# Performance work log

Hardware: AMD Instinct MI355X
Metric: run time of the kernel (lower is better)

## Reference

```python
import jax, jax.numpy as jnp
import numpy as np

# ---- config (YOLOv4-style, TRAIN_SIZE=608, P2..P5) ----
STRIDES = (4.0, 8.0, 16.0, 32.0)
ANCHORS = np.array([
    [[12, 16], [19, 36], [40, 28], [36, 75]],
    [[36, 75], [76, 55], [72, 146], [142, 110]],
    [[72, 146], [142, 110], [192, 243], [459, 401]],
    [[142, 110], [192, 243], [300, 300], [459, 401]],
], dtype=np.float32)  # [LEVELS, NUM_ANCHORS, 2]
MAX_PROP = 100
SCORE_THRESH = 0.25
IOU_THRESH = 0.5


def decode_prediction(p, anchors, stride):
    # p: [b, A, h, w, 6] -> [b, A*h*w, 5] with xyxy + score
    b, A, h, w, _ = p.shape
    txy, twh, conf, cls = p[..., :2], p[..., 2:4], p[..., 4:5], p[..., 5:6]
    gx, gy = jnp.meshgrid(jnp.arange(w, dtype=p.dtype), jnp.arange(h, dtype=p.dtype))
    grid = jnp.stack([gx, gy], axis=-1)[None, None]  # [1,1,h,w,2]
    xy = (jax.nn.sigmoid(txy) + grid) * stride
    wh = jnp.exp(twh) * anchors[None, :, None, None, :]
    score = jax.nn.sigmoid(conf) * jax.nn.sigmoid(cls)
    x1y1 = xy - 0.5 * wh
    x2y2 = xy + 0.5 * wh
    out = jnp.concatenate([x1y1, x2y2, score], axis=-1)  # [b,A,h,w,5]
    return out.reshape(b, A * h * w, 5)


def _iou_one_vs_all(box, boxes):
    # box: [4], boxes: [N,4] (xyxy)
    lt = jnp.maximum(box[:2], boxes[:, :2])
    rb = jnp.minimum(box[2:], boxes[:, 2:])
    wh = jnp.maximum(rb - lt, 0.0)
    inter = wh[:, 0] * wh[:, 1]
    a1 = jnp.maximum(box[2] - box[0], 0.0) * jnp.maximum(box[3] - box[1], 0.0)
    a2 = jnp.maximum(boxes[:, 2] - boxes[:, 0], 0.0) * jnp.maximum(boxes[:, 3] - boxes[:, 1], 0.0)
    return inter / (a1 + a2 - inter + 1e-9)


def _nms_single(boxes, scores):
    # greedy NMS, padded to MAX_PROP with zero rows
    s0 = jnp.where(scores >= SCORE_THRESH, scores, 0.0)

    def step(s, _):
        i = jnp.argmax(s)
        sc = s[i]
        box = boxes[i]
        keep = sc > 0.0
        row = jnp.where(keep, jnp.concatenate([box, sc[None]]), jnp.zeros(5, boxes.dtype))
        iou = _iou_one_vs_all(box, boxes)
        s = jnp.where((iou > IOU_THRESH) & keep, 0.0, s)
        s = s.at[i].set(0.0)
        return s, row

    _, props = jax.lax.scan(step, s0, None, length=MAX_PROP)
    return props  # [MAX_PROP, 5]


def entry_stop_gradients(t, mask):
    # gradient flows only through entries where mask==1
    return jax.lax.stop_gradient(t) * (1.0 - mask) + t * mask


def _forward(p2, p3, p4, p5):
    anchors = jnp.asarray(ANCHORS)
    d2 = decode_prediction(p2, anchors[0], STRIDES[0])
    d3 = decode_prediction(p3, anchors[1], STRIDES[1])
    d4 = decode_prediction(p4, anchors[2], STRIDES[2])
    d5 = decode_prediction(p5, anchors[3], STRIDES[3])
    proposals = jnp.concatenate([d2, d3, d4, d5], axis=1)  # [b, N, 5]
    proposals = jax.vmap(lambda pr: _nms_single(pr[:, :4], pr[:, 4]))(proposals)  # [b, MAX_PROP, 5]
    mask = (jnp.sum(proposals[..., :4], axis=-1) != 0.0).astype(proposals.dtype)[..., None]
    return entry_stop_gradients(proposals, mask)


def setup_inputs() -> dict:
    key = jax.random.key(0)
    k2, k3, k4, k5 = jax.random.split(key, 4)
    b, A, ch = 32, 4, 6
    return {
        "p2": jax.random.normal(k2, (b, A, 152, 152, ch), dtype=jnp.float32),
        "p3": jax.random.normal(k3, (b, A, 76, 76, ch), dtype=jnp.float32),
        "p4": jax.random.normal(k4, (b, A, 38, 38, ch), dtype=jnp.float32),
        "p5": jax.random.normal(k5, (b, A, 19, 19, ch), dtype=jnp.float32),
    }


def reference(p2, p3, p4, p5):
    return _forward(p2, p3, p4, p5)
```

## Files before the change

kernel.cpp:

```cpp
#include <hip/hip_runtime.h>
#include <cstdint>
#include <cstddef>

typedef unsigned int u32;
typedef unsigned long long u64;

#define NTOT 122740
#define NPAIR 61370
#define KTOP 1024
#define WIN  256
#define NBIN 4096
#define SCORE_T 0.25f
#define TBITS 0x3E800000u

#define RT0 0x3F5DF000u
#define RT1 0x3F3FF000u
#define RT2 0x3F1FF000u
#define RT3 0x3EFFF000u

#define CSTRIDE 128
#define CAP0 4096
#define CAP1 8192
#define CAP2 12288
#define CAP3 16384
#define CAP4 16384
#define OFF0 0
#define OFF1 4096
#define OFF2 12288
#define OFF3 24576
#define OFF4 40960
#define BATCH_ENT 57344

#define F4TOT 184110
#define F4B3 138624
#define F4B4 173280
#define F4B5 181944

#define F4_PER_BLK 3072

#define WS_CAND 16384

__device__ __forceinline__ float sigm(float x) { return 1.0f / (1.0f + expf(-x)); }

__device__ __forceinline__ int score_bin(u32 bits) {
  return min(4095, 1 + (int)((bits - TBITS) >> 12));
}

__device__ __forceinline__ u64 shfl_u64(u64 x, int src) {
  int lo = __shfl((int)(u32)x, src, 64);
  int hi = __shfl((int)(u32)(x >> 32), src, 64);
  return ((u64)(u32)hi << 32) | (u32)lo;
}

__device__ __forceinline__ void score_pair(int P, int b,
    const float* __restrict__ p2, const float* __restrict__ p3,
    const float* __restrict__ p4, const float* __restrict__ p5,
    u32& b0, u32& b1, u32& gi0, u32& gi1)
{
  int t0 = 2 * P;
  const float* p; int l0, LN;
  if (t0 < 92416)       { p = p2; l0 = t0;          LN = 92416; }
  else if (t0 < 115520) { p = p3; l0 = t0 - 92416;  LN = 23104; }
  else if (t0 < 121296) { p = p4; l0 = t0 - 115520; LN = 5776;  }
  else                  { p = p5; l0 = t0 - 121296; LN = 1444;  }
  const float* q = p + ((size_t)b * LN + (size_t)l0) * 6;
  float4 v1 = *(const float4*)(q + 4);
  float4 v2 = *(const float4*)(q + 8);
  float s0 = sigm(v1.x) * sigm(v1.y);
  float s1 = sigm(v2.z) * sigm(v2.w);
  b0 = (s0 >= SCORE_T) ? __float_as_uint(s0) : 0u;
  b1 = (s1 >= SCORE_T) ? __float_as_uint(s1) : 0u;
  gi0 = (u32)t0; gi1 = (u32)(t0 + 1);
}

__device__ float4 decode_box_from_gidx(u32 gidx, int b,
    const float* __restrict__ p2, const float* __restrict__ p3,
    const float* __restrict__ p4, const float* __restrict__ p5)
{
  const float* p; int t, H, W; float stride;
  float aw0, ah0, aw1, ah1, aw2, ah2, aw3, ah3;
  if (gidx < 92416u) {
    p = p2 + (size_t)b * 92416 * 6; t = (int)gidx; H = 152; W = 152; stride = 4.0f;
    aw0=12.f; ah0=16.f; aw1=19.f; ah1=36.f; aw2=40.f; ah2=28.f; aw3=36.f; ah3=75.f;
  } else if (gidx < 115520u) {
    p = p3 + (size_t)b * 23104 * 6; t = (int)(gidx - 92416u); H = 76; W = 76; stride = 8.0f;
    aw0=36.f; ah0=75.f; aw1=76.f; ah1=55.f; aw2=72.f; ah2=146.f; aw3=142.f; ah3=110.f;
  } else if (gidx < 121296u) {
    p = p4 + (size_t)b * 5776 * 6; t = (int)(gidx - 115520u); H = 38; W = 38; stride = 16.0f;
    aw0=72.f; ah0=146.f; aw1=142.f; ah1=110.f; aw2=192.f; ah2=243.f; aw3=459.f; ah3=401.f;
  } else {
    p = p5 + (size_t)b * 1444 * 6; t = (int)(gidx - 121296u); H = 19; W = 19; stride = 32.0f;
    aw0=142.f; ah0=110.f; aw1=192.f; ah1=243.f; aw2=300.f; ah2=300.f; aw3=459.f; ah3=401.f;
  }
  int HW = H * W;
  int a = t / HW;
  int r = t - a * HW;
  int y = r / W;
  int x = r - y * W;
  const float* q = p + (size_t)t * 6;
  float2 t01 = *(const float2*)(q + 0);
  float2 t23 = *(const float2*)(q + 2);
  float cx = (sigm(t01.x) + (float)x) * stride;
  float cy = (sigm(t01.y) + (float)y) * stride;
  float aw = (a == 0) ? aw0 : (a == 1) ? aw1 : (a == 2) ? aw2 : aw3;
  float ah = (a == 0) ? ah0 : (a == 1) ? ah1 : (a == 2) ? ah2 : ah3;
  float bw = expf(t23.x) * aw;
  float bh = expf(t23.y) * ah;
  return make_float4(cx - 0.5f * bw, cy - 0.5f * bh, cx + 0.5f * bw, cy + 0.5f * bh);
}

__device__ __forceinline__ bool iou_gt(float4 A, float4 B) {
  float ltx = fmaxf(A.x, B.x), lty = fmaxf(A.y, B.y);
  float rbx = fminf(A.z, B.z), rby = fminf(A.w, B.w);
  float w = fmaxf(rbx - ltx, 0.0f), h = fmaxf(rby - lty, 0.0f);
  float inter = w * h;
  float a1 = fmaxf(A.z - A.x, 0.0f) * fmaxf(A.w - A.y, 0.0f);
  float a2 = fmaxf(B.z - B.x, 0.0f) * fmaxf(B.w - B.y, 0.0f);
  float iou = inter / (a1 + a2 - inter + 1e-9f);
  return iou > 0.5f;
}

__global__ __launch_bounds__(512)
void decode_kernel(const float* __restrict__ p2, const float* __restrict__ p3,
                   const float* __restrict__ p4, const float* __restrict__ p5,
                   u32* __restrict__ counters, uint2* __restrict__ cand)
{
  __shared__ uint2 stg[2048];
  __shared__ u32 lcnt[8], lseg[8], lrank[8], gbase[8];
  const int tid = threadIdx.x;
  const int b = blockIdx.y;
  if (tid < 8) { lcnt[tid] = 0u; lrank[tid] = 0u; gbase[tid] = 0u; }
  __syncthreads();

  const float4* q2 = (const float4*)p2;
  const float4* q3 = (const float4*)p3;
  const float4* q4 = (const float4*)p4;
  const float4* q5 = (const float4*)p5;
  const int FS = blockIdx.x * F4_PER_BLK;

  u32 kb[6]; u32 kg6[6]; int kr6[6];
  #pragma unroll
  for (int k = 0; k < 6; ++k) {
    kb[k] = 0u; kr6[k] = -1; kg6[k] = 0u;
    int i4 = FS + k * 512 + tid;
    if (i4 < F4TOT) {
      const float4* src;
      if (i4 < F4B3)      src = q2 + (size_t)b * 138624 + i4;
      else if (i4 < F4B4) src = q3 + (size_t)b * 34656  + (i4 - F4B3);
      else if (i4 < F4B5) src = q4 + (size_t)b * 8664   + (i4 - F4B4);
      else                src = q5 + (size_t)b * 2166   + (i4 - F4B5);
      float4 v = *src;
      int k3 = i4 / 3;
      int trib = i4 - 3 * k3;
      if (trib) {
        float cf = (trib == 1) ? v.x : v.z;
        float cl = (trib == 1) ? v.y : v.w;
        float s = sigm(cf) * sigm(cl);
        if (s >= SCORE_T) {
          u32 bb = __float_as_uint(s);
          int r;
          if      (bb >= RT0) r = 0;
          else if (bb >= RT1) r = 1;
          else if (bb >= RT2) r = 2;
          else if (bb >= RT3) r = 3;
          else                r = 4;
          kb[k] = bb; kr6[k] = r;
          kg6[k] = (u32)(2 * k3 + (trib - 1));
          atomicAdd(&lcnt[r], 1u);
        }
      }
    }
  }
  __syncthreads();
  if (tid == 0) {
    u32 s = 0;
    #pragma unroll
    for (int r = 0; r < 5; ++r) { lseg[r] = s; s += lcnt[r]; }
  }
  if (tid < 5 && lcnt[tid]) gbase[tid] = atomicAdd(&counters[(size_t)b * CSTRIDE + tid * 16], lcnt[tid]);
  __syncthreads();
  #pragma unroll
  for (int k = 0; k < 6; ++k) {
    if (kr6[k] >= 0) {
      u32 rk = atomicAdd(&lrank[kr6[k]], 1u);
      stg[lseg[kr6[k]] + rk] = make_uint2(kb[k], kg6[k]);
    }
  }
  __syncthreads();
  uint2* cb = cand + (size_t)b * BATCH_ENT;
  const u32 roff[5] = { OFF0, OFF1, OFF2, OFF3, OFF4 };
  const u32 rcap[5] = { CAP0, CAP1, CAP2, CAP3, CAP4 };
  #pragma unroll
  for (int r = 0; r < 5; ++r) {
    const u32 cnt = lcnt[r], sg = lseg[r], gb = gbase[r];
    for (u32 i = tid; i < cnt; i += 512) {
      u32 d = gb + i;
      if (d < rcap[r]) cb[roff[r] + d] = stg[sg + i];
    }
  }
}

__global__ __launch_bounds__(1024, 1)
void mega_kernel(const u32* __restrict__ counters, const uint2* __restrict__ cand,
                 const float* __restrict__ p2, const float* __restrict__ p3,
                 const float* __restrict__ p4, const float* __restrict__ p5,
                 float* __restrict__ out)
{
  const int b = blockIdx.x;
  const int tid = threadIdx.x;
  const int lane = tid & 63, wv = tid >> 6;

  __shared__ __align__(16) u32 sstart[NBIN];
  __shared__ __align__(16) u32 scur[NBIN];
  __shared__ u32 wred[16];
  __shared__ u64 skey[KTOP];
  __shared__ u64 skey2[KTOP];
  __shared__ float4 sbox[WIN];
  __shared__ u64 smat[WIN * 4];
  __shared__ float4 selbox[100];
  __shared__ u32 s_sellist[100];
  __shared__ int s_misc[4];
  __shared__ int s_B, s_n;

  const u32 c0 = counters[(size_t)b * CSTRIDE +  0];
  const u32 c1 = counters[(size_t)b * CSTRIDE + 16];
  const u32 c2 = counters[(size_t)b * CSTRIDE + 32];
  const u32 c3 = counters[(size_t)b * CSTRIDE + 48];
  const u32 c4 = counters[(size_t)b * CSTRIDE + 64];
  const u32 total = c0 + c1 + c2 + c3 + c4;
  const u32 need = min((u32)KTOP, total);
  int RL = 0;
  { u32 cum = c0;
    if (cum < need) { RL = 1; cum += c1; }
    if (cum < need) { RL = 2; cum += c2; }
    if (cum < need) { RL = 3; cum += c3; }
    if (cum < need) { RL = 4; cum += c4; }
  }
  const bool fb = (c0 > (u32)CAP0)
               || (RL >= 1 && c1 > (u32)CAP1)
               || (RL >= 2 && c2 > (u32)CAP2)
               || (RL >= 3 && c3 > (u32)CAP3)
               || (RL >= 4 && c4 > (u32)CAP4);

  ((uint4*)scur)[tid] = make_uint4(0u, 0u, 0u, 0u);
  __syncthreads();

  const uint2* cb = cand + (size_t)b * BATCH_ENT;

  if (!fb) {
    for (u32 i = tid; i < c0; i += 1024) atomicAdd(&scur[score_bin(cb[OFF0 + i].x)], 1u);
    if (RL >= 1) for (u32 i = tid; i < c1; i += 1024) atomicAdd(&scur[score_bin(cb[OFF1 + i].x)], 1u);
    if (RL >= 2) for (u32 i = tid; i < c2; i += 1024) atomicAdd(&scur[score_bin(cb[OFF2 + i].x)], 1u);
    if (RL >= 3) for (u32 i = tid; i < c3; i += 1024) atomicAdd(&scur[score_bin(cb[OFF3 + i].x)], 1u);
    if (RL >= 4) for (u32 i = tid; i < c4; i += 1024) atomicAdd(&scur[score_bin(cb[OFF4 + i].x)], 1u);
  } else {
    for (int P = tid; P < NPAIR; P += 1024) {
      u32 b0, b1, gi0, gi1;
      score_pair(P, b, p2, p3, p4, p5, b0, b1, gi0, gi1);
      if (b0) atomicAdd(&scur[score_bin(b0)], 1u);
      if (b1) atomicAdd(&scur[score_bin(b1)], 1u);
    }
  }
  __syncthreads();

  {
    uint4 hv = ((const uint4*)scur)[tid];
    u32 loc4[4] = { hv.x, hv.y, hv.z, hv.w };
    u32 lsum = hv.x + hv.y + hv.z + hv.w;
    u32 S = lsum;
    #pragma unroll
    for (int off = 1; off < 64; off <<= 1) {
      u32 v = (u32)__shfl_down((int)S, off, 64);
      if (lane + off < 64) S += v;
    }
    u32 wtot = (u32)__shfl((int)S, 0, 64);
    if (lane == 0) wred[wv] = wtot;
    __syncthreads();
    u32 U = 0;
    for (int w2 = wv + 1; w2 < 16; ++w2) U += wred[w2];
    u32 T = U + (S - lsum);
    u32 ss[4];
    u32 run = T;
    #pragma unroll
    for (int j = 3; j >= 0; --j) { ss[j] = run; run += loc4[j]; }
    ((uint4*)sstart)[tid] = make_uint4(ss[0], ss[1], ss[2], ss[3]);
    u32 pk = 0xFFFFFFFFu;
    #pragma unroll
    for (int j = 0; j < 4; ++j) {
      u32 cge = ss[j] + loc4[j];
      if (pk == 0xFFFFFFFFu && cge <= (u32)KTOP) pk = ((u32)(4 * tid + j) << 12) | cge;
    }
    #pragma unroll
    for (int off = 32; off >= 1; off >>= 1) {
      u32 o = (u32)__shfl_down((int)pk, off, 64);
      if (lane + off < 64) pk = min(pk, o);
    }
    __syncthreads();
    if (lane == 0) wred[wv] = pk;
    __syncthreads();
    if (tid == 0) {
      u32 m = 0xFFFFFFFFu;
      for (int w2 = 0; w2 < 16; ++w2) m = min(m, wred[w2]);
      if (m == 0xFFFFFFFFu) { s_B = 4095; s_n = KTOP; }
      else { s_B = max((int)(m >> 12), 1); s_n = (int)(m & 0xFFFu); }
    }
  }
  __syncthreads();
  const int B = s_B;
  const int n = min(s_n, KTOP);

  ((uint4*)scur)[tid] = ((const uint4*)sstart)[tid];
  __syncthreads();

  if (!fb) {
    for (u32 i = tid; i < c0; i += 1024) {
      uint2 e = cb[OFF0 + i]; int bin = score_bin(e.x);
      if (bin >= B) { u32 sl = atomicAdd(&scur[bin], 1u);
        if (sl < (u32)KTOP) skey[sl] = ((u64)e.x << 32) | (u32)(~e.y); }
    }
    if (RL >= 1) for (u32 i = tid; i < c1; i += 1024) {
      uint2 e = cb[OFF1 + i]; int bin = score_bin(e.x);
      if (bin >= B) { u32 sl = atomicAdd(&scur[bin], 1u);
        if (sl < (u32)KTOP) skey[sl] = ((u64)e.x << 32) | (u32)(~e.y); }
    }
    if (RL >= 2) for (u32 i = tid; i < c2; i += 1024) {
      uint2 e = cb[OFF2 + i]; int bin = score_bin(e.x);
      if (bin >= B) { u32 sl = atomicAdd(&scur[bin], 1u);
        if (sl < (u32)KTOP) skey[sl] = ((u64)e.x << 32) | (u32)(~e.y); }
    }
    if (RL >= 3) for (u32 i = tid; i < c3; i += 1024) {
      uint2 e = cb[OFF3 + i]; int bin = score_bin(e.x);
      if (bin >= B) { u32 sl = atomicAdd(&scur[bin], 1u);
        if (sl < (u32)KTOP) skey[sl] = ((u64)e.x << 32) | (u32)(~e.y); }
    }
    if (RL >= 4) for (u32 i = tid; i < c4; i += 1024) {
      uint2 e = cb[OFF4 + i]; int bin = score_bin(e.x);
      if (bin >= B) { u32 sl = atomicAdd(&scur[bin], 1u);
        if (sl < (u32)KTOP) skey[sl] = ((u64)e.x << 32) | (u32)(~e.y); }
    }
  } else {
    for (int P = tid; P < NPAIR; P += 1024) {
      u32 b0, b1, gi0, gi1;
      score_pair(P, b, p2, p3, p4, p5, b0, b1, gi0, gi1);
      if (b0) { int bin = score_bin(b0);
        if (bin >= B) { u32 sl = atomicAdd(&scur[bin], 1u);
          if (sl < (u32)KTOP) skey[sl] = ((u64)b0 << 32) | (u32)(~gi0); } }
      if (b1) { int bin = score_bin(b1);
        if (bin >= B) { u32 sl = atomicAdd(&scur[bin], 1u);
          if (sl < (u32)KTOP) skey[sl] = ((u64)b1 << 32) | (u32)(~gi1); } }
    }
  }
  __syncthreads();

  for (int s = tid; s < n; s += 1024) {
    u64 k = skey[s];
    int bin = score_bin((u32)(k >> 32));
    int st = (int)sstart[bin];
    int en = (int)scur[bin];
    u32 r = 0;
    for (int j = st; j < en; ++j) r += (skey[j] > k) ? 1u : 0u;
    skey2[st + r] = k;
  }
  __syncthreads();

  const int Wn = min(n, WIN);

  if (tid < WIN) {
    sbox[tid] = (tid < Wn) ? decode_box_from_gidx(~(u32)skey2[tid], b, p2, p3, p4, p5)
                           : make_float4(0.f, 0.f, 0.f, 0.f);
  }
  __syncthreads();

  {
    int row = tid & 255, word = tid >> 8;
    u64 bits = 0;
    if (row < Wn) {
      float4 A = sbox[row];
      int j0 = word * 64;
      int je = min(64, Wn - j0);
      for (int j = 0; j < je; ++j)
        if (iou_gt(A, sbox[j0 + j])) bits |= (1ull << j);
    }
    smat[word * 256 + row] = bits;
  }
  __syncthreads();

  if (tid < 64) {
    u64 mA0 = smat[0*256 +   0 + lane], mA1 = smat[1*256 +   0 + lane],
        mA2 = smat[2*256 +   0 + lane], mA3 = smat[3*256 +   0 + lane];
    u64 mB0 = smat[0*256 +  64 + lane], mB1 = smat[1*256 +  64 + lane],
        mB2 = smat[2*256 +  64 + lane], mB3 = smat[3*256 +  64 + lane];
    u64 mC0 = smat[0*256 + 128 + lane], mC1 = smat[1*256 + 128 + lane],
        mC2 = smat[2*256 + 128 + lane], mC3 = smat[3*256 + 128 + lane];
    u64 mD0 = smat[0*256 + 192 + lane], mD1 = smat[1*256 + 192 + lane],
        mD2 = smat[2*256 + 192 + lane], mD3 = smat[3*256 + 192 + lane];

    u64 live0 = (Wn >=  64) ? ~0ull : (Wn >   0 ? ((1ull << (Wn -   0)) - 1ull) : 0ull);
    u64 live1 = (Wn >= 128) ? ~0ull : (Wn >  64 ? ((1ull << (Wn -  64)) - 1ull) : 0ull);
    u64 live2 = (Wn >= 192) ? ~0ull : (Wn > 128 ? ((1ull << (Wn - 128)) - 1ull) : 0ull);
    u64 live3 = (Wn >= 256) ? ~0ull : (Wn > 192 ? ((1ull << (Wn - 192)) - 1ull) : 0ull);
    int sel = 0;

    while (live0 && sel < 100) {
      int j = (int)__ffsll(live0) - 1;
      u64 r0 = shfl_u64(mA0, j), r1 = shfl_u64(mA1, j),
          r2 = shfl_u64(mA2, j), r3 = shfl_u64(mA3, j);
      live0 &= ~r0; live1 &= ~r1; live2 &= ~r2; live3 &= ~r3;
      live0 &= ~(1ull << j);
      if (lane == 0) s_sellist[sel] = (u32)j;
      sel++;
    }
    while (live1 && sel < 100) {
      int j = (int)__ffsll(live1) - 1;
      u64 r0 = shfl_u64(mB0, j), r1 = shfl_u64(mB1, j),
          r2 = shfl_u64(mB2, j), r3 = shfl_u64(mB3, j);
      live0 &= ~r0; live1 &= ~r1; live2 &= ~r2; live3 &= ~r3;
      live1 &= ~(1ull << j);
      if (lane == 0) s_sellist[sel] = (u32)(64 + j);
      sel++;
    }
    while (live2 && sel < 100) {
      int j = (int)__ffsll(live2) - 1;
      u64 r0 = shfl_u64(mC0, j), r1 = shfl_u64(mC1, j),
          r2 = shfl_u64(mC2, j), r3 = shfl_u64(mC3, j);
      live0 &= ~r0; live1 &= ~r1; live2 &= ~r2; live3 &= ~r3;
      live2 &= ~(1ull << j);
      if (lane == 0) s_sellist[sel] = (u32)(128 + j);
      sel++;
    }
    while (live3 && sel < 100) {
      int j = (int)__ffsll(live3) - 1;
      u64 r0 = shfl_u64(mD0, j), r1 = shfl_u64(mD1, j),
          r2 = shfl_u64(mD2, j), r3 = shfl_u64(mD3, j);
      live0 &= ~r0; live1 &= ~r1; live2 &= ~r2; live3 &= ~r3;
      live3 &= ~(1ull << j);
      if (lane == 0) s_sellist[sel] = (u32)(192 + j);
      sel++;
    }
    if (lane == 0) {
      s_misc[2] = sel;
      s_misc[3] = (sel < 100 && n > WIN) ? 1 : 0;
    }
  }
  __syncthreads();

  {
    const int nsel0 = s_misc[2];
    if (tid < nsel0) {
      int p = (int)s_sellist[tid];
      u64 k = skey2[p];
      float4 box = sbox[p];
      selbox[tid] = box;
      float* orow = out + (size_t)b * 500 + (size_t)tid * 5;
      orow[0] = box.x; orow[1] = box.y; orow[2] = box.z; orow[3] = box.w;
      orow[4] = __uint_as_float((u32)(k >> 32));
    }
  }
  __syncthreads();

  if (s_misc[3]) {
    if (tid < 64) {
      int sel = s_misc[2];
      for (int p = WIN; p < n && sel < 100; ++p) {
        u64 k = skey2[p];
        float4 box = decode_box_from_gidx(~(u32)k, b, p2, p3, p4, p5);
        bool hit = false;
        if (lane < sel) hit = iou_gt(selbox[lane], box);
        if (lane + 64 < sel) hit = hit || iou_gt(selbox[lane + 64], box);
        u64 anyhit = __ballot(hit);
        if (anyhit == 0ull) {
          if (lane == 0) {
            selbox[sel] = box;
            float sc = __uint_as_float((u32)(k >> 32));
            float* orow = out + (size_t)b * 500 + (size_t)sel * 5;
            orow[0] = box.x; orow[1] = box.y; orow[2] = box.z; orow[3] = box.w; orow[4] = sc;
          }
          sel++;
        }
      }
      if (lane == 0) s_misc[2] = sel;
    }
  }
  __syncthreads();

  const int nsel = s_misc[2];
  for (int i = tid; i < (100 - nsel) * 5; i += 1024)
    out[(size_t)b * 500 + (size_t)nsel * 5 + i] = 0.0f;
}

extern "C" void kernel_launch(void* const* d_in, const int* in_sizes, int n_in,
                              void* d_out, int out_size, void* d_ws, size_t ws_size,
                              hipStream_t stream) {
  const float* p2 = (const float*)d_in[0];
  const float* p3 = (const float*)d_in[1];
  const float* p4 = (const float*)d_in[2];
  const float* p5 = (const float*)d_in[3];
  float* out = (float*)d_out;

  unsigned char* w = (unsigned char*)d_ws;
  u32*   counters = (u32*)w;
  uint2* cand     = (uint2*)(w + WS_CAND);

  hipMemsetAsync(counters, 0, 32 * CSTRIDE * sizeof(u32), stream);
  decode_kernel<<<dim3(60, 32), 512, 0, stream>>>(p2, p3, p4, p5, counters, cand);
  mega_kernel<<<32, 1024, 0, stream>>>(counters, cand, p2, p3, p4, p5, out);
}
```

Before: 161.3 us.

## Write per-block candidate segments deterministically instead of global atomic bins

When the workspace is large enough, each decode block writes its staged candidates contiguously into a private segment and records per-range counts in a table, instead of reserving slots through global atomics into capped per-range buffers. The top-k kernel then sums the counts with a wave reduction and scans each block's prefix of needed ranges. This removes the counter memset and the global atomics, and it also removes the capacity-overflow fallback path. In exchange it uses more workspace, and the second kernel reads from 60 segments per batch.

```diff
diff --git a/kernel.cpp b/kernel.cpp
--- a/kernel.cpp
+++ b/kernel.cpp
@@ -30,15 +30,19 @@
 #define OFF3 24576
 #define OFF4 40960
 #define BATCH_ENT 57344
+#define WS_CAND_OLD 16384
+
+#define NREG 60
+#define REG_ENT 2048
+#define CNT_PAD 8
+#define WS_CANDDET 65536
+#define NEED_DET 31522816ull
 
 #define F4TOT 184110
 #define F4B3 138624
 #define F4B4 173280
 #define F4B5 181944
-
 #define F4_PER_BLK 3072
-
-#define WS_CAND 16384
 
 __device__ __forceinline__ float sigm(float x) { return 1.0f / (1.0f + expf(-x)); }
 
@@ -123,7 +127,9 @@
 __global__ __launch_bounds__(512)
 void decode_kernel(const float* __restrict__ p2, const float* __restrict__ p3,
                    const float* __restrict__ p4, const float* __restrict__ p5,
-                   u32* __restrict__ counters, uint2* __restrict__ cand)
+                   u32* __restrict__ counters, uint2* __restrict__ cand_old,
+                   u32* __restrict__ cnttab, uint2* __restrict__ cand_det,
+                   int det)
 {
   __shared__ uint2 stg[2048];
   __shared__ u32 lcnt[8], lseg[8], lrank[8], gbase[8];
@@ -177,7 +183,8 @@
     #pragma unroll
     for (int r = 0; r < 5; ++r) { lseg[r] = s; s += lcnt[r]; }
   }
-  if (tid < 5 && lcnt[tid]) gbase[tid] = atomicAdd(&counters[(size_t)b * CSTRIDE + tid * 16], lcnt[tid]);
+  if (!det && tid < 5 && lcnt[tid])
+    gbase[tid] = atomicAdd(&counters[(size_t)b * CSTRIDE + tid * 16], lcnt[tid]);
   __syncthreads();
   #pragma unroll
   for (int k = 0; k < 6; ++k) {
@@ -187,24 +194,33 @@
     }
   }
   __syncthreads();
-  uint2* cb = cand + (size_t)b * BATCH_ENT;
-  const u32 roff[5] = { OFF0, OFF1, OFF2, OFF3, OFF4 };
-  const u32 rcap[5] = { CAP0, CAP1, CAP2, CAP3, CAP4 };
-  #pragma unroll
-  for (int r = 0; r < 5; ++r) {
-    const u32 cnt = lcnt[r], sg = lseg[r], gb = gbase[r];
-    for (u32 i = tid; i < cnt; i += 512) {
-      u32 d = gb + i;
-      if (d < rcap[r]) cb[roff[r] + d] = stg[sg + i];
+
+  if (det) {
+    if (tid < 5) cnttab[((size_t)b * NREG + blockIdx.x) * CNT_PAD + tid] = lcnt[tid];
+    const u32 tot = lseg[4] + lcnt[4];
+    uint2* cb = cand_det + ((size_t)b * NREG + blockIdx.x) * REG_ENT;
+    for (u32 i = tid; i < tot; i += 512) cb[i] = stg[i];
+  } else {
+    uint2* cb = cand_old + (size_t)b * BATCH_ENT;
+    const u32 roff[5] = { OFF0, OFF1, OFF2, OFF3, OFF4 };
+    const u32 rcap[5] = { CAP0, CAP1, CAP2, CAP3, CAP4 };
+    #pragma unroll
+    for (int r = 0; r < 5; ++r) {
+      const u32 cnt = lcnt[r], sg = lseg[r], gb = gbase[r];
+      for (u32 i = tid; i < cnt; i += 512) {
+        u32 d = gb + i;
+        if (d < rcap[r]) cb[roff[r] + d] = stg[sg + i];
+      }
     }
   }
 }
 
 __global__ __launch_bounds__(1024, 1)
-void mega_kernel(const u32* __restrict__ counters, const uint2* __restrict__ cand,
+void mega_kernel(const u32* __restrict__ counters, const uint2* __restrict__ cand_old,
+                 const u32* __restrict__ cnttab, const uint2* __restrict__ cand_det,
                  const float* __restrict__ p2, const float* __restrict__ p3,
                  const float* __restrict__ p4, const float* __restrict__ p5,
-                 float* __restrict__ out)
+                 float* __restrict__ out, int det)
 {
   const int b = blockIdx.x;
   const int tid = threadIdx.x;
@@ -213,6 +229,7 @@
   __shared__ __align__(16) u32 sstart[NBIN];
   __shared__ __align__(16) u32 scur[NBIN];
   __shared__ u32 wred[16];
+  __shared__ u32 s_plen[NREG + 4];
   __shared__ u64 skey[KTOP];
   __shared__ u64 skey2[KTOP];
   __shared__ float4 sbox[WIN];
@@ -222,32 +239,75 @@
   __shared__ int s_misc[4];
   __shared__ int s_B, s_n;
 
-  const u32 c0 = counters[(size_t)b * CSTRIDE +  0];
-  const u32 c1 = counters[(size_t)b * CSTRIDE + 16];
-  const u32 c2 = counters[(size_t)b * CSTRIDE + 32];
-  const u32 c3 = counters[(size_t)b * CSTRIDE + 48];
-  const u32 c4 = counters[(size_t)b * CSTRIDE + 64];
-  const u32 total = c0 + c1 + c2 + c3 + c4;
-  const u32 need = min((u32)KTOP, total);
-  int RL = 0;
-  { u32 cum = c0;
-    if (cum < need) { RL = 1; cum += c1; }
-    if (cum < need) { RL = 2; cum += c2; }
-    if (cum < need) { RL = 3; cum += c3; }
-    if (cum < need) { RL = 4; cum += c4; }
-  }
-  const bool fb = (c0 > (u32)CAP0)
-               || (RL >= 1 && c1 > (u32)CAP1)
-               || (RL >= 2 && c2 > (u32)CAP2)
-               || (RL >= 3 && c3 > (u32)CAP3)
-               || (RL >= 4 && c4 > (u32)CAP4);
-
   ((uint4*)scur)[tid] = make_uint4(0u, 0u, 0u, 0u);
-  __syncthreads();
-
-  const uint2* cb = cand + (size_t)b * BATCH_ENT;
-
-  if (!fb) {
+
+  u32 c0, c1, c2, c3, c4; int RL; bool fb = false;
+  if (det) {
+    if (tid < 64) {
+      u32 m0 = 0, m1 = 0, m2 = 0, m3 = 0, m4 = 0;
+      if (lane < NREG) {
+        const u32* t = cnttab + ((size_t)b * NREG + lane) * CNT_PAD;
+        m0 = t[0]; m1 = t[1]; m2 = t[2]; m3 = t[3]; m4 = t[4];
+      }
+      u32 r0 = m0, r1 = m1, r2 = m2, r3 = m3, r4 = m4;
+      #pragma unroll
+      for (int off = 32; off >= 1; off >>= 1) {
+        r0 += (u32)__shfl_down((int)r0, off, 64);
+        r1 += (u32)__shfl_down((int)r1, off, 64);
+        r2 += (u32)__shfl_down((int)r2, off, 64);
+        r3 += (u32)__shfl_down((int)r3, off, 64);
+        r4 += (u32)__shfl_down((int)r4, off, 64);
+      }
+      u32 t0 = (u32)__shfl((int)r0, 0, 64), t1 = (u32)__shfl((int)r1, 0, 64);
+      u32 t2 = (u32)__shfl((int)r2, 0, 64), t3 = (u32)__shfl((int)r3, 0, 64);
+      u32 t4 = (u32)__shfl((int)r4, 0, 64);
+      u32 total = t0 + t1 + t2 + t3 + t4;
+      u32 need = min((u32)KTOP, total);
+      int rl = 0; u32 cum = t0;
+      if (cum < need) { rl = 1; cum += t1; }
+      if (cum < need) { rl = 2; cum += t2; }
+      if (cum < need) { rl = 3; cum += t3; }
+      if (cum < need) { rl = 4; cum += t4; }
+      u32 pl = m0;
+      if (rl >= 1) pl += m1;
+      if (rl >= 2) pl += m2;
+      if (rl >= 3) pl += m3;
+      if (rl >= 4) pl += m4;
+      if (lane < NREG) s_plen[lane] = pl;
+    }
+    __syncthreads();
+  } else {
+    c0 = counters[(size_t)b * CSTRIDE +  0];
+    c1 = counters[(size_t)b * CSTRIDE + 16];
+    c2 = counters[(size_t)b * CSTRIDE + 32];
+    c3 = counters[(size_t)b * CSTRIDE + 48];
+    c4 = counters[(size_t)b * CSTRIDE + 64];
+    const u32 total = c0 + c1 + c2 + c3 + c4;
+    const u32 need = min((u32)KTOP, total);
+    RL = 0;
+    { u32 cum = c0;
+      if (cum < need) { RL = 1; cum += c1; }
+      if (cum < need) { RL = 2; cum += c2; }
+      if (cum < need) { RL = 3; cum += c3; }
+      if (cum < need) { RL = 4; cum += c4; }
+    }
+    fb = (c0 > (u32)CAP0)
+      || (RL >= 1 && c1 > (u32)CAP1)
+      || (RL >= 2 && c2 > (u32)CAP2)
+      || (RL >= 3 && c3 > (u32)CAP3)
+      || (RL >= 4 && c4 > (u32)CAP4);
+    __syncthreads();
+  }
+
+  const uint2* cb = cand_old + (size_t)b * BATCH_ENT;
+
+  if (det) {
+    for (int sg = wv; sg < NREG; sg += 16) {
+      const u32 len = s_plen[sg];
+      const uint2* seg = cand_det + ((size_t)b * NREG + sg) * REG_ENT;
+      for (u32 i = lane; i < len; i += 64) atomicAdd(&scur[score_bin(seg[i].x)], 1u);
+    }
+  } else if (!fb) {
     for (u32 i = tid; i < c0; i += 1024) atomicAdd(&scur[score_bin(cb[OFF0 + i].x)], 1u);
     if (RL >= 1) for (u32 i = tid; i < c1; i += 1024) atomicAdd(&scur[score_bin(cb[OFF1 + i].x)], 1u);
     if (RL >= 2) for (u32 i = tid; i < c2; i += 1024) atomicAdd(&scur[score_bin(cb[OFF2 + i].x)], 1u);
@@ -312,7 +372,17 @@
   ((uint4*)scur)[tid] = ((const uint4*)sstart)[tid];
   __syncthreads();
 
-  if (!fb) {
+  if (det) {
+    for (int sg = wv; sg < NREG; sg += 16) {
+      const u32 len = s_plen[sg];
+      const uint2* seg = cand_det + ((size_t)b * NREG + sg) * REG_ENT;
+      for (u32 i = lane; i < len; i += 64) {
+        uint2 e = seg[i]; int bin = score_bin(e.x);
+        if (bin >= B) { u32 sl = atomicAdd(&scur[bin], 1u);
+          if (sl < (u32)KTOP) skey[sl] = ((u64)e.x << 32) | (u32)(~e.y); }
+      }
+    }
+  } else if (!fb) {
     for (u32 i = tid; i < c0; i += 1024) {
       uint2 e = cb[OFF0 + i]; int bin = score_bin(e.x);
       if (bin >= B) { u32 sl = atomicAdd(&scur[bin], 1u);
@@ -499,9 +569,15 @@
 
   unsigned char* w = (unsigned char*)d_ws;
   u32*   counters = (u32*)w;
-  uint2* cand     = (uint2*)(w + WS_CAND);
-
-  hipMemsetAsync(counters, 0, 32 * CSTRIDE * sizeof(u32), stream);
-  decode_kernel<<<dim3(60, 32), 512, 0, stream>>>(p2, p3, p4, p5, counters, cand);
-  mega_kernel<<<32, 1024, 0, stream>>>(counters, cand, p2, p3, p4, p5, out);
-}
+  uint2* cand_old = (uint2*)(w + WS_CAND_OLD);
+  u32*   cnttab   = (u32*)w;
+  uint2* cand_det = (uint2*)(w + WS_CANDDET);
+
+  const int det = (ws_size >= (size_t)NEED_DET) ? 1 : 0;
+  if (!det) hipMemsetAsync(counters, 0, 32 * CSTRIDE * sizeof(u32), stream);
+  decode_kernel<<<dim3(NREG, 32), 512, 0, stream>>>(p2, p3, p4, p5,
+                                                    counters, cand_old,
+                                                    cnttab, cand_det, det);
+  mega_kernel<<<32, 1024, 0, stream>>>(counters, cand_old, cnttab, cand_det,
+                                       p2, p3, p4, p5, out, det);
+}
```

Result: no change. 160.0 us (-0.8%).
